# Optimization experiments

Measured on AMD Instinct MI355X. Metric: run time of the kernel, lower is better.

## Reference

```python
import jax, jax.numpy as jnp
import numpy as np

V, E, H, L = 32000, 512, 1024, 2
B, S, T = 32, 64, 64


def setup_inputs() -> dict:
    key = jax.random.key(0)
    ks = jax.random.split(key, 16)
    sd = 0.05
    p = lambda k, shape: (jax.random.normal(k, shape, jnp.float32) * sd)
    z = lambda shape: jnp.zeros(shape, jnp.float32)
    return {
        "tgt_batch": jax.random.randint(ks[0], (B, S), 0, V),
        "enc_h": p(ks[1], (L, B, H)),
        "enc_c": p(ks[2], (L, B, H)),
        "enc_outputs": p(ks[3], (T, B, H)),
        "emb": p(ks[4], (V, E)),
        "W_ih0": p(ks[5], (4 * H, E + H)),
        "W_hh0": p(ks[6], (4 * H, H)),
        "b_ih0": z((4 * H,)),
        "b_hh0": z((4 * H,)),
        "W_ih1": p(ks[7], (4 * H, H)),
        "W_hh1": p(ks[8], (4 * H, H)),
        "b_ih1": z((4 * H,)),
        "b_hh1": z((4 * H,)),
        "Wa": p(ks[9], (H, 2 * H)),
        "ba": z((H,)),
        "va": p(ks[10], (H,)),
        "Wc": p(ks[11], (H, 2 * H)),
        "bc": z((H,)),
        "Wo": p(ks[12], (V, H)),
        "bo": z((V,)),
        "teacher_forcing": 1,
    }


def _lstm_cell(x, h, c, Wih, Whh, bih, bhh):
    # PyTorch gate order: i, f, g, o
    g = x @ Wih.T + bih + h @ Whh.T + bhh
    i, f, gg, o = jnp.split(g, 4, axis=1)
    c2 = jax.nn.sigmoid(f) * c + jax.nn.sigmoid(i) * jnp.tanh(gg)
    return jax.nn.sigmoid(o) * jnp.tanh(c2), c2


def reference(tgt_batch, enc_h, enc_c, enc_outputs, emb,
              W_ih0, W_hh0, b_ih0, b_hh0, W_ih1, W_hh1, b_ih1, b_hh1,
              Wa, ba, va, Wc, bc, Wo, bo, teacher_forcing):
    # teacher_forcing == 1 -> always feed the gold previous word (matches
    # the torch loop, whose sampling branch is never taken at tf=1.0).
    tgt = tgt_batch.T  # [S, B], seq-first

    def step(carry, x_t):
        h, c, attn_h = carry  # h,c: [L,B,H]; attn_h: [B,H]
        x = jnp.concatenate([emb[x_t], attn_h], axis=1)  # [B, E+H]
        h0, c0 = _lstm_cell(x, h[0], c[0], W_ih0, W_hh0, b_ih0, b_hh0)
        h1, c1 = _lstm_cell(h0, h[1], c[1], W_ih1, W_hh1, b_ih1, b_hh1)
        # additive ('concat') attention over encoder states, query = top h
        hid = jnp.broadcast_to(h1[None], enc_outputs.shape)  # [T,B,H]
        energy = jnp.tanh(jnp.concatenate([hid, enc_outputs], axis=-1) @ Wa.T + ba)
        scores = jnp.einsum('tbh,h->bt', energy, va)  # [B,T]
        weights = jax.nn.softmax(scores, axis=1)
        context = jnp.einsum('bt,tbh->bh', weights, enc_outputs)  # [B,H]
        attn_h2 = jnp.tanh(jnp.concatenate([h1, context], axis=1) @ Wc.T + bc)
        logp = jax.nn.log_softmax(attn_h2 @ Wo.T + bo, axis=1)  # [B,V]
        return (jnp.stack([h0, h1]), jnp.stack([c0, c1]), attn_h2), logp

    init = (enc_h, enc_c, jnp.zeros((tgt.shape[1], H), enc_h.dtype))
    _, dec_outputs = jax.lax.scan(step, init, tgt[:-1])  # [S-1, B, V]
    dec_output_words = jnp.argmax(dec_outputs, axis=-1).astype(jnp.int32)
    return dec_outputs, dec_output_words
```

## Files before the change

kernel.cpp:

```cpp
#include <hip/hip_runtime.h>
#include <math.h>

#define VOCAB 32000
#define EMBD  512
#define HID   1024
#define BATCH 32
#define SEQ   64
#define TENC  64
#define NSTEP 63
#define G4    4096

typedef __attribute__((ext_vector_type(8))) short short8;
typedef __attribute__((ext_vector_type(4))) float f32x4;
typedef __attribute__((ext_vector_type(4))) unsigned short us4;
typedef unsigned short u16;

__device__ __forceinline__ float4 ld4(const float* p) {
  return *reinterpret_cast<const float4*>(p);
}
__device__ __forceinline__ u16 f2bf(float x) {
  unsigned u = __float_as_uint(x);
  return (u16)((u + 0x7fffu + ((u >> 16) & 1u)) >> 16);
}
__device__ __forceinline__ float bf2f(u16 h) {
  return __uint_as_float(((unsigned)h) << 16);
}

template<int MODE>
__device__ __forceinline__ void mfma32(
    const u16* __restrict__ Xahi, const u16* __restrict__ Xalo,
    const u16* __restrict__ Xbhi, const u16* __restrict__ Xblo,
    const u16* __restrict__ Whi,  const u16* __restrict__ Wlo,
    int nt, float* res)
{
  const int tid = threadIdx.x;
  const int w = tid >> 6, l = tid & 63;
  const int c = l & 15, koct = l >> 4;
  constexpr int K   = (MODE == 0) ? 2048 : 1024;
  constexpr int WS  = (MODE == 0) ? 2048 : 1024;
  constexpr int SPW = K / 32 / 4;
  const int r0 = c, r1 = 16 + c;
  const int wr0 = (MODE == 0) ? ((r0 >> 3)*1024 + nt*8 + (r0 & 7)) : (nt*32 + r0);
  const int wr1 = (MODE == 0) ? ((r1 >> 3)*1024 + nt*8 + (r1 & 7)) : (nt*32 + r1);
  const u16* bh0 = Whi + (size_t)wr0 * WS;
  const u16* bh1 = Whi + (size_t)wr1 * WS;
  const u16* bl0 = Wlo + (size_t)wr0 * WS;
  const u16* bl1 = Wlo + (size_t)wr1 * WS;

  auto ldA = [&](int m, int kg, int lo) -> short8 {
    const u16* base;
    if (MODE == 0 && kg >= 1024) base = lo ? Xblo : Xbhi;
    else                         base = lo ? Xalo : Xahi;
    const int b = m*16 + c;
    return *reinterpret_cast<const short8*>(base + b*1024 + (kg & 1023));
  };

  f32x4 acc[2][2];
  #pragma unroll
  for (int m = 0; m < 2; ++m)
    #pragma unroll
    for (int n = 0; n < 2; ++n) acc[m][n] = (f32x4){0.f,0.f,0.f,0.f};

  const int s0 = w * SPW;
  short8 Ah[2], Al[2], Bh[2], Bl[2];
  {
    const int kg = s0*32 + koct*8;
    Ah[0]=ldA(0,kg,0); Ah[1]=ldA(1,kg,0); Al[0]=ldA(0,kg,1); Al[1]=ldA(1,kg,1);
    Bh[0]=*reinterpret_cast<const short8*>(bh0+kg);
    Bh[1]=*reinterpret_cast<const short8*>(bh1+kg);
    Bl[0]=*reinterpret_cast<const short8*>(bl0+kg);
    Bl[1]=*reinterpret_cast<const short8*>(bl1+kg);
  }
  for (int s = s0; s < s0 + SPW; ++s) {
    short8 nAh[2], nAl[2], nBh[2], nBl[2];
    if (s + 1 < s0 + SPW) {
      const int kg = (s+1)*32 + koct*8;
      nAh[0]=ldA(0,kg,0); nAh[1]=ldA(1,kg,0); nAl[0]=ldA(0,kg,1); nAl[1]=ldA(1,kg,1);
      nBh[0]=*reinterpret_cast<const short8*>(bh0+kg);
      nBh[1]=*reinterpret_cast<const short8*>(bh1+kg);
      nBl[0]=*reinterpret_cast<const short8*>(bl0+kg);
      nBl[1]=*reinterpret_cast<const short8*>(bl1+kg);
    }
    #pragma unroll
    for (int n = 0; n < 2; ++n)
      #pragma unroll
      for (int m = 0; m < 2; ++m) {
        acc[m][n] = __builtin_amdgcn_mfma_f32_16x16x32_bf16(Ah[m], Bh[n], acc[m][n], 0, 0, 0);
        acc[m][n] = __builtin_amdgcn_mfma_f32_16x16x32_bf16(Ah[m], Bl[n], acc[m][n], 0, 0, 0);
        acc[m][n] = __builtin_amdgcn_mfma_f32_16x16x32_bf16(Al[m], Bh[n], acc[m][n], 0, 0, 0);
      }
    #pragma unroll
    for (int i = 0; i < 2; ++i) { Ah[i]=nAh[i]; Al[i]=nAl[i]; Bh[i]=nBh[i]; Bl[i]=nBl[i]; }
  }
  #pragma unroll
  for (int m = 0; m < 2; ++m)
    #pragma unroll
    for (int n = 0; n < 2; ++n)
      #pragma unroll
      for (int r = 0; r < 4; ++r) {
        const int b = m*16 + koct*4 + r;
        const int rr = n*16 + c;
        res[w*1056 + b*33 + rr] = acc[m][n][r];
      }
}

struct GKM {
  const u16 *Xahi, *Xalo, *Xbhi, *Xblo;
  const u16 *Whi, *Wlo;
  const float* bsum; const float* gembt;
  float* c; u16 *hhi; u16 *hlo;
};

template<int HASGEMB>
__global__ __launch_bounds__(256) void gates_mfma_k(GKM P) {
  __shared__ float res[4*1056];
  mfma32<0>(P.Xahi, P.Xalo, P.Xbhi, P.Xblo, P.Whi, P.Wlo, blockIdx.x, res);
  __syncthreads();
  const int tid = threadIdx.x;
  const int b = tid >> 3, j = tid & 7;
  const int n = blockIdx.x*8 + j;
  float g4[4];
  #pragma unroll
  for (int g = 0; g < 4; ++g) {
    const int r = g*8 + j;
    float s = P.bsum[g*1024 + n]
            + res[b*33+r] + res[1056 + b*33+r] + res[2112 + b*33+r] + res[3168 + b*33+r];
    if (HASGEMB) s += P.gembt[(size_t)b*G4 + g*1024 + n];
    g4[g] = s;
  }
  const float si = 1.f/(1.f+expf(-g4[0]));
  const float sf = 1.f/(1.f+expf(-g4[1]));
  const float so = 1.f/(1.f+expf(-g4[3]));
  const int i = b*HID + n;
  const float cn = sf*P.c[i] + si*tanhf(g4[2]);
  P.c[i] = cn;
  const float h = so*tanhf(cn);
  const u16 hh = f2bf(h);
  P.hhi[i] = hh;
  P.hlo[i] = f2bf(h - bf2f(hh));
}

struct PKM {
  const u16 *Xhi, *Xlo; const u16 *Whi, *Wlo; float* Pq;
};

__global__ __launch_bounds__(256) void proj_mfma_k(PKM P) {
  __shared__ float res[4*1056];
  mfma32<1>(P.Xhi, P.Xlo, nullptr, nullptr, P.Whi, P.Wlo, blockIdx.x, res);
  __syncthreads();
  const int tid = threadIdx.x;
  #pragma unroll
  for (int q = 0; q < 4; ++q) {
    const int o = q*256 + tid;
    const int b = o >> 5, r = o & 31;
    const float s = res[b*33+r] + res[1056 + b*33+r]
                  + res[2112 + b*33+r] + res[3168 + b*33+r];
    P.Pq[(size_t)b*2048 + blockIdx.x*32 + r] = s;
  }
}

struct AKM {
  const float* Pq; const float* PreAC; const float* va; const float* bc;
  u16* AHthi; u16* AHtlo;
};

__global__ __launch_bounds__(1024) void attn_k(AKM P) {
  __shared__ float QS[HID];
  __shared__ float sw[TENC];
  __shared__ float W64[TENC];
  const int b = blockIdx.x;
  const int tid = threadIdx.x;
  QS[tid] = P.Pq[(size_t)b*2048 + tid];
  __syncthreads();
  const int lane = tid & 63, wid = tid >> 6;
  float vreg[16];
  #pragma unroll
  for (int i2 = 0; i2 < 16; ++i2) vreg[i2] = P.va[lane + 64*i2];
  #pragma unroll
  for (int j = 0; j < 4; ++j) {
    const int te = wid*4 + j;
    const float* pr = P.PreAC + ((size_t)te*BATCH + b)*2048;
    float s = 0.f;
    #pragma unroll
    for (int i2 = 0; i2 < 16; ++i2) {
      const int idx = lane + 64*i2;
      s += vreg[i2] * tanhf(QS[idx] + pr[idx]);
    }
    #pragma unroll
    for (int off = 32; off; off >>= 1) s += __shfl_xor(s, off);
    if (lane == 0) sw[te] = s;
  }
  __syncthreads();
  if (tid < TENC) {
    const float v = sw[tid];
    float mx = v;
    #pragma unroll
    for (int off = 32; off; off >>= 1) mx = fmaxf(mx, __shfl_xor(mx, off));
    const float e = expf(v - mx);
    float sum = e;
    #pragma unroll
    for (int off = 32; off; off >>= 1) sum += __shfl_xor(sum, off);
    W64[tid] = e / sum;
  }
  __syncthreads();
  const int hh = tid;
  float acc = 0.f;
  #pragma unroll 8
  for (int te = 0; te < TENC; ++te)
    acc += W64[te] * P.PreAC[((size_t)te*BATCH + b)*2048 + HID + hh];
  const float hc = P.Pq[(size_t)b*2048 + HID + hh] + P.bc[hh];
  const float ah = tanhf(acc + hc);
  const u16 ahh = f2bf(ah);
  P.AHthi[(size_t)b*HID + hh] = ahh;
  P.AHtlo[(size_t)b*HID + hh] = f2bf(ah - bf2f(ahh));
}

struct TM {
  const u16 *Ahi, *Alo, *Bhi, *Blo;
  const int* tgt; const float* bias;
  float* out; int ldc, M, ntile_n;
};

template<int NC, int AMODE>
__global__ __launch_bounds__(256) void tile_k(TM P) {
  __shared__ float smemf[6144];
  u16* sA = (u16*)smemf;
  u16* sB = sA + 4096;
  constexpr int K = NC * 32;
  const int tile = blockIdx.x;
  const int mi = tile / P.ntile_n, ni = tile % P.ntile_n;
  const int m0 = mi * 64, n0 = ni * 128;
  const int tid = threadIdx.x;
  const int w = tid >> 6, l = tid & 63;
  const int mb = (w & 1) * 32, nb = (w >> 1) * 64;
  f32x4 acc[2][4];
  #pragma unroll
  for (int mt = 0; mt < 2; ++mt)
    #pragma unroll
    for (int nt = 0; nt < 4; ++nt) acc[mt][nt] = (f32x4){0.f,0.f,0.f,0.f};

  const int arow = tid >> 2, akg = tid & 3;
  const int brow = tid >> 1, bkg = (tid & 1) * 2;
  size_t arbase;
  if (AMODE == 1) {
    const int row = m0 + arow;
    const int tok = P.tgt[(row & 31)*SEQ + (row >> 5)];
    arbase = (size_t)tok * K;
  } else {
    arbase = (size_t)(m0 + arow) * K;
  }
  const size_t brbase = (size_t)(n0 + brow) * K;

  short8 pah, pal, pbh0, pbh1, pbl0, pbl1;
  {
    const size_t ao = arbase + akg*8;
    const size_t bo0 = brbase + bkg*8;
    pah  = *reinterpret_cast<const short8*>(P.Ahi + ao);
    pal  = *reinterpret_cast<const short8*>(P.Alo + ao);
    pbh0 = *reinterpret_cast<const short8*>(P.Bhi + bo0);
    pbh1 = *reinterpret_cast<const short8*>(P.Bhi + bo0 + 8);
    pbl0 = *reinterpret_cast<const short8*>(P.Blo + bo0);
    pbl1 = *reinterpret_cast<const short8*>(P.Blo + bo0 + 8);
  }
  for (int kc = 0; kc < NC; ++kc) {
    __syncthreads();
    *reinterpret_cast<short8*>(sA + ((0*4 + akg)*64 + arow)*8) = pah;
    *reinterpret_cast<short8*>(sA + ((1*4 + akg)*64 + arow)*8) = pal;
    *reinterpret_cast<short8*>(sB + ((0*4 + bkg  )*128 + brow)*8) = pbh0;
    *reinterpret_cast<short8*>(sB + ((0*4 + bkg+1)*128 + brow)*8) = pbh1;
    *reinterpret_cast<short8*>(sB + ((1*4 + bkg  )*128 + brow)*8) = pbl0;
    *reinterpret_cast<short8*>(sB + ((1*4 + bkg+1)*128 + brow)*8) = pbl1;
    __syncthreads();
    if (kc + 1 < NC) {
      const size_t ao = arbase + (kc+1)*32 + akg*8;
      const size_t bo0 = brbase + (kc+1)*32 + bkg*8;
      pah  = *reinterpret_cast<const short8*>(P.Ahi + ao);
      pal  = *reinterpret_cast<const short8*>(P.Alo + ao);
      pbh0 = *reinterpret_cast<const short8*>(P.Bhi + bo0);
      pbh1 = *reinterpret_cast<const short8*>(P.Bhi + bo0 + 8);
      pbl0 = *reinterpret_cast<const short8*>(P.Blo + bo0);
      pbl1 = *reinterpret_cast<const short8*>(P.Blo + bo0 + 8);
    }
    const int kg = l >> 4, rr = l & 15;
    short8 ah[2], al[2];
    #pragma unroll
    for (int mt = 0; mt < 2; ++mt) {
      ah[mt] = *reinterpret_cast<const short8*>(sA + ((0*4 + kg)*64 + mb + mt*16 + rr)*8);
      al[mt] = *reinterpret_cast<const short8*>(sA + ((1*4 + kg)*64 + mb + mt*16 + rr)*8);
    }
    #pragma unroll
    for (int nt = 0; nt < 4; ++nt) {
      const short8 bh = *reinterpret_cast<const short8*>(sB + ((0*4 + kg)*128 + nb + nt*16 + rr)*8);
      const short8 bl = *reinterpret_cast<const short8*>(sB + ((1*4 + kg)*128 + nb + nt*16 + rr)*8);
      #pragma unroll
      for (int mt = 0; mt < 2; ++mt) {
        acc[mt][nt] = __builtin_amdgcn_mfma_f32_16x16x32_bf16(ah[mt], bh, acc[mt][nt], 0, 0, 0);
        acc[mt][nt] = __builtin_amdgcn_mfma_f32_16x16x32_bf16(ah[mt], bl, acc[mt][nt], 0, 0, 0);
        acc[mt][nt] = __builtin_amdgcn_mfma_f32_16x16x32_bf16(al[mt], bh, acc[mt][nt], 0, 0, 0);
      }
    }
  }
  #pragma unroll
  for (int mt = 0; mt < 2; ++mt) {
    #pragma unroll
    for (int nt = 0; nt < 4; ++nt) {
      #pragma unroll
      for (int r = 0; r < 4; ++r) {
        const int row = m0 + mb + mt*16 + (l >> 4)*4 + r;
        const int col = n0 + nb + nt*16 + (l & 15);
        if (row < P.M) {
          const float bb = P.bias ? P.bias[col] : 0.f;
          P.out[(size_t)row*P.ldc + col] = acc[mt][nt][r] + bb;
        }
      }
    }
  }
}

template<int MODE>
__global__ __launch_bounds__(256) void pack_k(const float* __restrict__ A,
                                              const float* __restrict__ B,
                                              u16* __restrict__ hi, u16* __restrict__ lo) {
  constexpr int ROWS = (MODE == 2 || MODE == 3) ? 2048 : 4096;
  constexpr int K    = (MODE == 2 || MODE == 3) ? 1024 : (MODE == 4 ? 512 : 2048);
  const size_t total = (size_t)ROWS * (K/4);
  for (size_t i = (size_t)blockIdx.x*256 + threadIdx.x; i < total;
       i += (size_t)gridDim.x*256) {
    const int row = (int)(i / (K/4));
    const int k = (int)(i % (K/4)) * 4;
    float4 v;
    if (MODE == 0) v = (k < 1024) ? ld4(A + (size_t)row*1536 + 512 + k)
                                  : ld4(B + (size_t)row*1024 + (k - 1024));
    else if (MODE == 1) v = (k < 1024) ? ld4(A + (size_t)row*1024 + k)
                                       : ld4(B + (size_t)row*1024 + (k - 1024));
    else if (MODE == 2) v = (row < 1024) ? ld4(A + (size_t)row*2048 + k)
                                         : ld4(B + (size_t)(row - 1024)*2048 + k);
    else if (MODE == 3) v = (row < 1024) ? ld4(A + (size_t)row*2048 + 1024 + k)
                                         : ld4(B + (size_t)(row - 1024)*2048 + 1024 + k);
    else v = ld4(A + (size_t)row*1536 + k);
    us4 h, l;
    h.x = f2bf(v.x); l.x = f2bf(v.x - bf2f(h.x));
    h.y = f2bf(v.y); l.y = f2bf(v.y - bf2f(h.y));
    h.z = f2bf(v.z); l.z = f2bf(v.z - bf2f(h.z));
    h.w = f2bf(v.w); l.w = f2bf(v.w - bf2f(h.w));
    *reinterpret_cast<us4*>(hi + i*4) = h;
    *reinterpret_cast<us4*>(lo + i*4) = l;
  }
}

__global__ __launch_bounds__(256) void cvt_k(const float* __restrict__ src,
                                             u16* __restrict__ hi,
                                             u16* __restrict__ lo, int n) {
  int i = (blockIdx.x*256 + threadIdx.x) * 4;
  const int stride = gridDim.x * 256 * 4;
  for (; i < n; i += stride) {
    const float4 v = ld4(src + i);
    us4 h, l;
    h.x = f2bf(v.x); l.x = f2bf(v.x - bf2f(h.x));
    h.y = f2bf(v.y); l.y = f2bf(v.y - bf2f(h.y));
    h.z = f2bf(v.z); l.z = f2bf(v.z - bf2f(h.z));
    h.w = f2bf(v.w); l.w = f2bf(v.w - bf2f(h.w));
    *reinterpret_cast<us4*>(hi + i) = h;
    *reinterpret_cast<us4*>(lo + i) = l;
  }
}

struct WGP {
  const float* A; const float* W; const float* W2; const float* bias;
  const int* tgt; const float* emb;
  float* C; int ldc;
};

template<int WM>
__device__ __forceinline__ float4 ldWL(const WGP& P, int r, int k) {
  if (WM == 2) return ld4(P.W + (size_t)r * (EMBD + HID) + k);
  if (r < HID) return ld4(P.W  + (size_t)r * (2*HID) + HID + k);
  return ld4(P.W2 + (size_t)(r - HID) * (2*HID) + HID + k);
}

template<int WM>
__device__ __forceinline__ float4 ldAL(const WGP& P, int row, int k) {
  if (WM == 2) {
    const int tok = P.tgt[(row & 31) * SEQ + (row >> 5)];
    return ld4(P.emb + (size_t)tok * EMBD + k);
  }
  return ld4(P.A + (size_t)row * 1024 + k);
}

template<int WM>
__global__ __launch_bounds__(256, 2) void gemmL(WGP P) {
  constexpr int KK = (WM == 2) ? 512 : 1024;
  __shared__ float At[32*36];
  __shared__ float Wt[32*260];
  const int tid = threadIdx.x;
  const int m0 = blockIdx.x * 32;
  const int n0 = blockIdx.y * 256;
  const int lr = tid >> 3, lc = (tid & 7) << 2;
  const int tn = tid & 31, tm = tid >> 5;
  float acc[4][8];
  #pragma unroll
  for (int i = 0; i < 4; ++i)
    #pragma unroll
    for (int x = 0; x < 8; ++x) acc[i][x] = 0.f;

  float4 av = ldAL<WM>(P, m0 + lr, lc);
  float4 wv[8];
  #pragma unroll
  for (int it = 0; it < 8; ++it) wv[it] = ldWL<WM>(P, n0 + lr + it*32, lc);

  for (int k0 = 0; k0 < KK; k0 += 32) {
    float4 avn, wvn[8];
    if (k0 + 32 < KK) {
      avn = ldAL<WM>(P, m0 + lr, k0 + 32 + lc);
      #pragma unroll
      for (int it = 0; it < 8; ++it) wvn[it] = ldWL<WM>(P, n0 + lr + it*32, k0 + 32 + lc);
    }
    __syncthreads();
    At[(lc+0)*36+lr]=av.x; At[(lc+1)*36+lr]=av.y; At[(lc+2)*36+lr]=av.z; At[(lc+3)*36+lr]=av.w;
    #pragma unroll
    for (int it = 0; it < 8; ++it) {
      const int r = lr + it*32;
      Wt[(lc+0)*260+r]=wv[it].x; Wt[(lc+1)*260+r]=wv[it].y;
      Wt[(lc+2)*260+r]=wv[it].z; Wt[(lc+3)*260+r]=wv[it].w;
    }
    __syncthreads();
    #pragma unroll
    for (int kk = 0; kk < 32; ++kk) {
      const float4 a  = *reinterpret_cast<const float4*>(&At[kk*36 + tm*4]);
      const float4 w0 = *reinterpret_cast<const float4*>(&Wt[kk*260 + tn*8]);
      const float4 w1 = *reinterpret_cast<const float4*>(&Wt[kk*260 + tn*8 + 4]);
      #pragma unroll
      for (int i = 0; i < 4; ++i) {
        const float ai = (&a.x)[i];
        acc[i][0]+=ai*w0.x; acc[i][1]+=ai*w0.y; acc[i][2]+=ai*w0.z; acc[i][3]+=ai*w0.w;
        acc[i][4]+=ai*w1.x; acc[i][5]+=ai*w1.y; acc[i][6]+=ai*w1.z; acc[i][7]+=ai*w1.w;
      }
    }
    av = avn;
    #pragma unroll
    for (int it = 0; it < 8; ++it) wv[it] = wvn[it];
  }
  const int na = n0 + tn*8, ma = m0 + tm*4;
  float bb[8];
  #pragma unroll
  for (int x = 0; x < 8; ++x) {
    if (WM == 1) bb[x] = (na + x < HID) ? P.bias[na+x] : 0.f;
    else         bb[x] = 0.f;
  }
  #pragma unroll
  for (int i = 0; i < 4; ++i)
    #pragma unroll
    for (int x = 0; x < 8; ++x)
      P.C[(size_t)(ma+i)*P.ldc + na + x] = acc[i][x] + bb[x];
}

__global__ __launch_bounds__(512) void lsm_k(float* __restrict__ out,
                                             float* __restrict__ words) {
  const int b = blockIdx.x;
  const int t = blockIdx.y;
  float* row = out + ((size_t)t*BATCH + b)*VOCAB;
  const int tid = threadIdx.x;
  float m = -INFINITY, s = 0.f; int mi = 0;
  for (int v = tid; v < VOCAB; v += 512) {
    const float x = row[v];
    if (x > m) { s = s * expf(m - x) + 1.f; m = x; mi = v; }
    else s += expf(x - m);
  }
  __shared__ float sm[512]; __shared__ float sv[512]; __shared__ int si[512];
  sm[tid] = m; sv[tid] = s; si[tid] = mi;
  __syncthreads();
  for (int st = 256; st; st >>= 1) {
    if (tid < st) {
      const float om = sm[tid+st], os = sv[tid+st]; const int oi = si[tid+st];
      if (om > sm[tid]) {
        sv[tid] = os + sv[tid] * expf(sm[tid] - om);
        sm[tid] = om; si[tid] = oi;
      } else if (om == sm[tid]) {
        sv[tid] += os;
        if (oi < si[tid]) si[tid] = oi;
      } else {
        sv[tid] += os * expf(om - sm[tid]);
      }
    }
    __syncthreads();
  }
  const float lse = logf(sv[0]) + sm[0];
  const int amax = si[0];
  for (int v = tid; v < VOCAB; v += 512) row[v] = row[v] - lse;
  if (tid == 0) words[(size_t)t*BATCH + b] = (float)amax;
}

__global__ __launch_bounds__(256) void init_k(const float* __restrict__ enc_h,
                                              const float* __restrict__ enc_c,
                                              const float* __restrict__ bih0,
                                              const float* __restrict__ bhh0,
                                              const float* __restrict__ bih1,
                                              const float* __restrict__ bhh1,
                                              const float* __restrict__ ba,
                                              float* c0, float* c1,
                                              u16* h0hi, u16* h0lo, u16* h1hi, u16* h1lo,
                                              u16* zahhi, u16* zahlo,
                                              float* bsum0, float* bsum1,
                                              float* bias2048) {
  const int i = blockIdx.x*256 + threadIdx.x;
  if (i < BATCH*HID) {
    c0[i] = enc_c[i]; c1[i] = enc_c[BATCH*HID + i];
    const float v0 = enc_h[i];
    const u16 h0 = f2bf(v0);
    h0hi[i] = h0; h0lo[i] = f2bf(v0 - bf2f(h0));
    const float v1 = enc_h[BATCH*HID + i];
    const u16 h1 = f2bf(v1);
    h1hi[i] = h1; h1lo[i] = f2bf(v1 - bf2f(h1));
    zahhi[i] = 0; zahlo[i] = 0;
  }
  if (i < G4) {
    bsum0[i] = bih0[i] + bhh0[i];
    bsum1[i] = bih1[i] + bhh1[i];
  }
  if (i < 2048) bias2048[i] = (i < HID) ? ba[i] : 0.f;
}

extern "C" void kernel_launch(void* const* d_in, const int* in_sizes, int n_in,
                              void* d_out, int out_size, void* d_ws, size_t ws_size,
                              hipStream_t stream) {
  const int*   tgt   = (const int*)d_in[0];
  const float* enc_h = (const float*)d_in[1];
  const float* enc_c = (const float*)d_in[2];
  const float* enc   = (const float*)d_in[3];
  const float* emb   = (const float*)d_in[4];
  const float* Wih0  = (const float*)d_in[5];
  const float* Whh0  = (const float*)d_in[6];
  const float* bih0  = (const float*)d_in[7];
  const float* bhh0  = (const float*)d_in[8];
  const float* Wih1  = (const float*)d_in[9];
  const float* Whh1  = (const float*)d_in[10];
  const float* bih1  = (const float*)d_in[11];
  const float* bhh1  = (const float*)d_in[12];
  const float* Wa    = (const float*)d_in[13];
  const float* ba    = (const float*)d_in[14];
  const float* va    = (const float*)d_in[15];
  const float* Wc    = (const float*)d_in[16];
  const float* bc    = (const float*)d_in[17];
  const float* Wo    = (const float*)d_in[18];
  const float* bo    = (const float*)d_in[19];

  char* base = (char*)d_ws;
  size_t cur = 0;
  auto take = [&](size_t bytes) { char* p = base + cur; cur = (cur + bytes + 63) & ~(size_t)63; return p; };

  u16* AHhi = (u16*)take((size_t)2048*1024*2);
  u16* AHlo = (u16*)take((size_t)2048*1024*2);
  float* PreAC = (float*)take((size_t)2048*2048*4);
  float* Gemb  = (float*)take((size_t)NSTEP*BATCH*G4*4);
  float* Pq    = (float*)take((size_t)BATCH*2048*4);
  float* c0    = (float*)take(BATCH*HID*4);
  float* c1v   = (float*)take(BATCH*HID*4);
  float* bsum0 = (float*)take(G4*4);
  float* bsum1 = (float*)take(G4*4);
  float* bias2048 = (float*)take(2048*4);
  u16* W0hi = (u16*)take((size_t)4096*2048*2);
  u16* W0lo = (u16*)take((size_t)4096*2048*2);
  u16* W1hi = (u16*)take((size_t)4096*2048*2);
  u16* W1lo = (u16*)take((size_t)4096*2048*2);
  u16* WAhi = (u16*)take((size_t)2048*1024*2);
  u16* WAlo = (u16*)take((size_t)2048*1024*2);
  u16* h0Ahi = (u16*)take(BATCH*HID*2);
  u16* h0Alo = (u16*)take(BATCH*HID*2);
  u16* h0Bhi = (u16*)take(BATCH*HID*2);
  u16* h0Blo = (u16*)take(BATCH*HID*2);
  u16* h1Ahi = (u16*)take(BATCH*HID*2);
  u16* h1Alo = (u16*)take(BATCH*HID*2);
  u16* h1Bhi = (u16*)take(BATCH*HID*2);
  u16* h1Blo = (u16*)take(BATCH*HID*2);
  u16* zahhi = (u16*)take(BATCH*HID*2);
  u16* zahlo = (u16*)take(BATCH*HID*2);
  char* S = take((size_t)VOCAB*1024*2*2);
  const bool fast = ws_size >= cur;

  u16* enchi = (u16*)S;
  u16* enclo = enchi + (size_t)2048*1024;
  u16* embhi = enclo + (size_t)2048*1024;
  u16* emblo = embhi + (size_t)VOCAB*EMBD;
  u16* WAChi = emblo + (size_t)VOCAB*EMBD;
  u16* WAClo = WAChi + (size_t)2048*1024;
  u16* W0ehi = WAClo + (size_t)2048*1024;
  u16* W0elo = W0ehi + (size_t)4096*512;
  u16* Wohi = fast ? (u16*)S : (u16*)PreAC;
  u16* Wolo = Wohi + (size_t)VOCAB*1024;

  float* out   = (float*)d_out;
  float* words = out + (size_t)NSTEP*BATCH*VOCAB;

  init_k<<<dim3(128), 256, 0, stream>>>(enc_h, enc_c, bih0, bhh0, bih1, bhh1, ba,
                                        c0, c1v, h0Ahi, h0Alo, h1Ahi, h1Alo,
                                        zahhi, zahlo, bsum0, bsum1, bias2048);

  if (fast) {
    cvt_k<<<dim3(512), 256, 0, stream>>>(enc, enchi, enclo, 2048*1024);
    cvt_k<<<dim3(4096), 256, 0, stream>>>(emb, embhi, emblo, VOCAB*EMBD);
    pack_k<3><<<dim3(512), 256, 0, stream>>>(Wa, Wc, WAChi, WAClo);
    pack_k<4><<<dim3(512), 256, 0, stream>>>(Wih0, nullptr, W0ehi, W0elo);
    {
      TM p; p.Ahi = enchi; p.Alo = enclo; p.Bhi = WAChi; p.Blo = WAClo;
      p.tgt = nullptr; p.bias = bias2048; p.out = PreAC;
      p.ldc = 2048; p.M = 2048; p.ntile_n = 16;
      tile_k<32,0><<<dim3(512), 256, 0, stream>>>(p);
    }
    {
      TM p; p.Ahi = embhi; p.Alo = emblo; p.Bhi = W0ehi; p.Blo = W0elo;
      p.tgt = tgt; p.bias = nullptr; p.out = Gemb;
      p.ldc = G4; p.M = NSTEP*BATCH; p.ntile_n = 32;
      tile_k<16,1><<<dim3(1024), 256, 0, stream>>>(p);
    }
  } else {
    { WGP p = {}; p.A = enc; p.W = Wa; p.W2 = Wc; p.bias = ba; p.C = PreAC; p.ldc = 2048;
      gemmL<1><<<dim3(64, 8), 256, 0, stream>>>(p); }
    { WGP p = {}; p.W = Wih0; p.tgt = tgt; p.emb = emb; p.C = Gemb; p.ldc = G4;
      gemmL<2><<<dim3(NSTEP*BATCH/32, G4/256), 256, 0, stream>>>(p); }
  }
  pack_k<0><<<dim3(1024), 256, 0, stream>>>(Wih0, Whh0, W0hi, W0lo);
  pack_k<1><<<dim3(1024), 256, 0, stream>>>(Wih1, Whh1, W1hi, W1lo);
  pack_k<2><<<dim3(512), 256, 0, stream>>>(Wa, Wc, WAhi, WAlo);

  for (int t = 0; t < NSTEP; ++t) {
    const u16* ahphi = t ? (AHhi + (size_t)(t-1)*BATCH*HID) : zahhi;
    const u16* ahplo = t ? (AHlo + (size_t)(t-1)*BATCH*HID) : zahlo;
    const u16* h0phi = (t & 1) ? h0Bhi : h0Ahi;
    const u16* h0plo = (t & 1) ? h0Blo : h0Alo;
    u16* h0chi = (t & 1) ? h0Ahi : h0Bhi;
    u16* h0clo = (t & 1) ? h0Alo : h0Blo;
    const u16* h1phi = (t & 1) ? h1Bhi : h1Ahi;
    const u16* h1plo = (t & 1) ? h1Blo : h1Alo;
    u16* h1chi = (t & 1) ? h1Ahi : h1Bhi;
    u16* h1clo = (t & 1) ? h1Alo : h1Blo;

    {
      GKM p = {};
      p.Xahi = ahphi; p.Xalo = ahplo; p.Xbhi = h0phi; p.Xblo = h0plo;
      p.Whi = W0hi; p.Wlo = W0lo;
      p.bsum = bsum0; p.gembt = Gemb + (size_t)t*BATCH*G4;
      p.c = c0; p.hhi = h0chi; p.hlo = h0clo;
      gates_mfma_k<1><<<dim3(128), 256, 0, stream>>>(p);
    }
    {
      GKM p = {};
      p.Xahi = h0chi; p.Xalo = h0clo; p.Xbhi = h1phi; p.Xblo = h1plo;
      p.Whi = W1hi; p.Wlo = W1lo;
      p.bsum = bsum1; p.gembt = nullptr;
      p.c = c1v; p.hhi = h1chi; p.hlo = h1clo;
      gates_mfma_k<0><<<dim3(128), 256, 0, stream>>>(p);
    }
    {
      PKM p; p.Xhi = h1chi; p.Xlo = h1clo; p.Whi = WAhi; p.Wlo = WAlo; p.Pq = Pq;
      proj_mfma_k<<<dim3(64), 256, 0, stream>>>(p);
    }
    {
      AKM p; p.Pq = Pq; p.PreAC = PreAC; p.va = va; p.bc = bc;
      p.AHthi = AHhi + (size_t)t*BATCH*HID;
      p.AHtlo = AHlo + (size_t)t*BATCH*HID;
      attn_k<<<dim3(BATCH), 1024, 0, stream>>>(p);
    }
  }

  cvt_k<<<dim3(4096), 256, 0, stream>>>(Wo, Wohi, Wolo, VOCAB*1024);
  {
    TM p; p.Ahi = AHhi; p.Alo = AHlo; p.Bhi = Wohi; p.Blo = Wolo;
    p.tgt = nullptr; p.bias = bo; p.out = out;
    p.ldc = VOCAB; p.M = NSTEP*BATCH; p.ntile_n = 250;
    tile_k<32,0><<<dim3(8000), 256, 0, stream>>>(p);
  }
  lsm_k<<<dim3(BATCH, NSTEP), 512, 0, stream>>>(out, words);
}
```

Measured before the change: 6.062 ms.

## Split recurrent GEMM K-loop across 8 waves and merge prep kernels into one launch

The per-step gates and projection MFMA kernels now use 512 threads (8 waves) per block, splitting the K dimension across twice as many waves and reducing the partial sums from shared memory. This targets the latency-bound sequential recurrence, where only 128 or 64 blocks run per step, by raising per-block parallelism. Separately, the weight and activation conversion and packing kernels are merged into a single prep launch dispatched by block index, cutting launch count. The cost is more shared memory per block and a longer reduction step.

```diff
diff --git a/kernel.cpp b/kernel.cpp
--- a/kernel.cpp
+++ b/kernel.cpp
@@ -26,7 +26,7 @@
   return __uint_as_float(((unsigned)h) << 16);
 }
 
-template<int MODE>
+template<int MODE, int NW>
 __device__ __forceinline__ void mfma32(
     const u16* __restrict__ Xahi, const u16* __restrict__ Xalo,
     const u16* __restrict__ Xbhi, const u16* __restrict__ Xblo,
@@ -38,7 +38,7 @@
   const int c = l & 15, koct = l >> 4;
   constexpr int K   = (MODE == 0) ? 2048 : 1024;
   constexpr int WS  = (MODE == 0) ? 2048 : 1024;
-  constexpr int SPW = K / 32 / 4;
+  constexpr int SPW = K / 32 / NW;
   const int r0 = c, r1 = 16 + c;
   const int wr0 = (MODE == 0) ? ((r0 >> 3)*1024 + nt*8 + (r0 & 7)) : (nt*32 + r0);
   const int wr1 = (MODE == 0) ? ((r1 >> 3)*1024 + nt*8 + (r1 & 7)) : (nt*32 + r1);
@@ -112,49 +112,53 @@
 };
 
 template<int HASGEMB>
-__global__ __launch_bounds__(256) void gates_mfma_k(GKM P) {
-  __shared__ float res[4*1056];
-  mfma32<0>(P.Xahi, P.Xalo, P.Xbhi, P.Xblo, P.Whi, P.Wlo, blockIdx.x, res);
+__global__ __launch_bounds__(512) void gates_mfma_k(GKM P) {
+  __shared__ float res[8*1056];
+  mfma32<0,8>(P.Xahi, P.Xalo, P.Xbhi, P.Xblo, P.Whi, P.Wlo, blockIdx.x, res);
   __syncthreads();
   const int tid = threadIdx.x;
-  const int b = tid >> 3, j = tid & 7;
-  const int n = blockIdx.x*8 + j;
-  float g4[4];
-  #pragma unroll
-  for (int g = 0; g < 4; ++g) {
-    const int r = g*8 + j;
-    float s = P.bsum[g*1024 + n]
-            + res[b*33+r] + res[1056 + b*33+r] + res[2112 + b*33+r] + res[3168 + b*33+r];
-    if (HASGEMB) s += P.gembt[(size_t)b*G4 + g*1024 + n];
-    g4[g] = s;
-  }
-  const float si = 1.f/(1.f+expf(-g4[0]));
-  const float sf = 1.f/(1.f+expf(-g4[1]));
-  const float so = 1.f/(1.f+expf(-g4[3]));
-  const int i = b*HID + n;
-  const float cn = sf*P.c[i] + si*tanhf(g4[2]);
-  P.c[i] = cn;
-  const float h = so*tanhf(cn);
-  const u16 hh = f2bf(h);
-  P.hhi[i] = hh;
-  P.hlo[i] = f2bf(h - bf2f(hh));
+  if (tid < 256) {
+    const int b = tid >> 3, j = tid & 7;
+    const int n = blockIdx.x*8 + j;
+    float g4[4];
+    #pragma unroll
+    for (int g = 0; g < 4; ++g) {
+      const int r = g*8 + j;
+      float s = P.bsum[g*1024 + n];
+      #pragma unroll
+      for (int w = 0; w < 8; ++w) s += res[w*1056 + b*33 + r];
+      if (HASGEMB) s += P.gembt[(size_t)b*G4 + g*1024 + n];
+      g4[g] = s;
+    }
+    const float si = 1.f/(1.f+expf(-g4[0]));
+    const float sf = 1.f/(1.f+expf(-g4[1]));
+    const float so = 1.f/(1.f+expf(-g4[3]));
+    const int i = b*HID + n;
+    const float cn = sf*P.c[i] + si*tanhf(g4[2]);
+    P.c[i] = cn;
+    const float h = so*tanhf(cn);
+    const u16 hh = f2bf(h);
+    P.hhi[i] = hh;
+    P.hlo[i] = f2bf(h - bf2f(hh));
+  }
 }
 
 struct PKM {
   const u16 *Xhi, *Xlo; const u16 *Whi, *Wlo; float* Pq;
 };
 
-__global__ __launch_bounds__(256) void proj_mfma_k(PKM P) {
-  __shared__ float res[4*1056];
-  mfma32<1>(P.Xhi, P.Xlo, nullptr, nullptr, P.Whi, P.Wlo, blockIdx.x, res);
+__global__ __launch_bounds__(512) void proj_mfma_k(PKM P) {
+  __shared__ float res[8*1056];
+  mfma32<1,8>(P.Xhi, P.Xlo, nullptr, nullptr, P.Whi, P.Wlo, blockIdx.x, res);
   __syncthreads();
   const int tid = threadIdx.x;
   #pragma unroll
-  for (int q = 0; q < 4; ++q) {
-    const int o = q*256 + tid;
+  for (int q = 0; q < 2; ++q) {
+    const int o = q*512 + tid;
     const int b = o >> 5, r = o & 31;
-    const float s = res[b*33+r] + res[1056 + b*33+r]
-                  + res[2112 + b*33+r] + res[3168 + b*33+r];
+    float s = 0.f;
+    #pragma unroll
+    for (int w = 0; w < 8; ++w) s += res[w*1056 + b*33 + r];
     P.Pq[(size_t)b*2048 + blockIdx.x*32 + r] = s;
   }
 }
@@ -317,15 +321,32 @@
   }
 }
 
+__device__ __forceinline__ void cvt_body(const float* __restrict__ src,
+                                         u16* __restrict__ hi, u16* __restrict__ lo,
+                                         int n, int bid, int nblk) {
+  int i = (bid*256 + (int)threadIdx.x) * 4;
+  const int stride = nblk * 256 * 4;
+  for (; i < n; i += stride) {
+    const float4 v = ld4(src + i);
+    us4 h, l;
+    h.x = f2bf(v.x); l.x = f2bf(v.x - bf2f(h.x));
+    h.y = f2bf(v.y); l.y = f2bf(v.y - bf2f(h.y));
+    h.z = f2bf(v.z); l.z = f2bf(v.z - bf2f(h.z));
+    h.w = f2bf(v.w); l.w = f2bf(v.w - bf2f(h.w));
+    *reinterpret_cast<us4*>(hi + i) = h;
+    *reinterpret_cast<us4*>(lo + i) = l;
+  }
+}
+
 template<int MODE>
-__global__ __launch_bounds__(256) void pack_k(const float* __restrict__ A,
-                                              const float* __restrict__ B,
-                                              u16* __restrict__ hi, u16* __restrict__ lo) {
+__device__ __forceinline__ void pk_body(const float* __restrict__ A,
+                                        const float* __restrict__ B,
+                                        u16* __restrict__ hi, u16* __restrict__ lo,
+                                        int bid, int nblk) {
   constexpr int ROWS = (MODE == 2 || MODE == 3) ? 2048 : 4096;
   constexpr int K    = (MODE == 2 || MODE == 3) ? 1024 : (MODE == 4 ? 512 : 2048);
   const size_t total = (size_t)ROWS * (K/4);
-  for (size_t i = (size_t)blockIdx.x*256 + threadIdx.x; i < total;
-       i += (size_t)gridDim.x*256) {
+  for (size_t i = (size_t)bid*256 + threadIdx.x; i < total; i += (size_t)nblk*256) {
     const int row = (int)(i / (K/4));
     const int k = (int)(i % (K/4)) * 4;
     float4 v;
@@ -348,21 +369,34 @@
   }
 }
 
+struct PrepP {
+  const float *enc, *emb, *Wa, *Wc, *Wih0, *Whh0, *Wih1, *Whh1;
+  u16 *enchi,*enclo,*embhi,*emblo,*WAChi,*WAClo,*W0ehi,*W0elo;
+  u16 *W0hi,*W0lo,*W1hi,*W1lo,*WAhi,*WAlo;
+};
+
+template<int FAST>
+__global__ __launch_bounds__(256) void prep_k(PrepP P) {
+  const int bid = blockIdx.x;
+  if (FAST) {
+    if      (bid < 256)  cvt_body(P.enc, P.enchi, P.enclo, 2048*1024, bid, 256);
+    else if (bid < 2304) cvt_body(P.emb, P.embhi, P.emblo, VOCAB*EMBD, bid-256, 2048);
+    else if (bid < 2560) pk_body<3>(P.Wa, P.Wc, P.WAChi, P.WAClo, bid-2304, 256);
+    else if (bid < 2816) pk_body<4>(P.Wih0, nullptr, P.W0ehi, P.W0elo, bid-2560, 256);
+    else if (bid < 3840) pk_body<0>(P.Wih0, P.Whh0, P.W0hi, P.W0lo, bid-2816, 1024);
+    else if (bid < 4864) pk_body<1>(P.Wih1, P.Whh1, P.W1hi, P.W1lo, bid-3840, 1024);
+    else                 pk_body<2>(P.Wa, P.Wc, P.WAhi, P.WAlo, bid-4864, 256);
+  } else {
+    if      (bid < 1024) pk_body<0>(P.Wih0, P.Whh0, P.W0hi, P.W0lo, bid, 1024);
+    else if (bid < 2048) pk_body<1>(P.Wih1, P.Whh1, P.W1hi, P.W1lo, bid-1024, 1024);
+    else                 pk_body<2>(P.Wa, P.Wc, P.WAhi, P.WAlo, bid-2048, 256);
+  }
+}
+
 __global__ __launch_bounds__(256) void cvt_k(const float* __restrict__ src,
                                              u16* __restrict__ hi,
                                              u16* __restrict__ lo, int n) {
-  int i = (blockIdx.x*256 + threadIdx.x) * 4;
-  const int stride = gridDim.x * 256 * 4;
-  for (; i < n; i += stride) {
-    const float4 v = ld4(src + i);
-    us4 h, l;
-    h.x = f2bf(v.x); l.x = f2bf(v.x - bf2f(h.x));
-    h.y = f2bf(v.y); l.y = f2bf(v.y - bf2f(h.y));
-    h.z = f2bf(v.z); l.z = f2bf(v.z - bf2f(h.z));
-    h.w = f2bf(v.w); l.w = f2bf(v.w - bf2f(h.w));
-    *reinterpret_cast<us4*>(hi + i) = h;
-    *reinterpret_cast<us4*>(lo + i) = l;
-  }
+  cvt_body(src, hi, lo, n, blockIdx.x, gridDim.x);
 }
 
 struct WGP {
@@ -595,11 +629,19 @@
                                         c0, c1v, h0Ahi, h0Alo, h1Ahi, h1Alo,
                                         zahhi, zahlo, bsum0, bsum1, bias2048);
 
+  {
+    PrepP p;
+    p.enc = enc; p.emb = emb; p.Wa = Wa; p.Wc = Wc;
+    p.Wih0 = Wih0; p.Whh0 = Whh0; p.Wih1 = Wih1; p.Whh1 = Whh1;
+    p.enchi = enchi; p.enclo = enclo; p.embhi = embhi; p.emblo = emblo;
+    p.WAChi = WAChi; p.WAClo = WAClo; p.W0ehi = W0ehi; p.W0elo = W0elo;
+    p.W0hi = W0hi; p.W0lo = W0lo; p.W1hi = W1hi; p.W1lo = W1lo;
+    p.WAhi = WAhi; p.WAlo = WAlo;
+    if (fast) prep_k<1><<<dim3(5120), 256, 0, stream>>>(p);
+    else      prep_k<0><<<dim3(2304), 256, 0, stream>>>(p);
+  }
+
   if (fast) {
-    cvt_k<<<dim3(512), 256, 0, stream>>>(enc, enchi, enclo, 2048*1024);
-    cvt_k<<<dim3(4096), 256, 0, stream>>>(emb, embhi, emblo, VOCAB*EMBD);
-    pack_k<3><<<dim3(512), 256, 0, stream>>>(Wa, Wc, WAChi, WAClo);
-    pack_k<4><<<dim3(512), 256, 0, stream>>>(Wih0, nullptr, W0ehi, W0elo);
     {
       TM p; p.Ahi = enchi; p.Alo = enclo; p.Bhi = WAChi; p.Blo = WAClo;
       p.tgt = nullptr; p.bias = bias2048; p.out = PreAC;
@@ -618,9 +660,6 @@
     { WGP p = {}; p.W = Wih0; p.tgt = tgt; p.emb = emb; p.C = Gemb; p.ldc = G4;
       gemmL<2><<<dim3(NSTEP*BATCH/32, G4/256), 256, 0, stream>>>(p); }
   }
-  pack_k<0><<<dim3(1024), 256, 0, stream>>>(Wih0, Whh0, W0hi, W0lo);
-  pack_k<1><<<dim3(1024), 256, 0, stream>>>(Wih1, Whh1, W1hi, W1lo);
-  pack_k<2><<<dim3(512), 256, 0, stream>>>(Wa, Wc, WAhi, WAlo);
 
   for (int t = 0; t < NSTEP; ++t) {
     const u16* ahphi = t ? (AHhi + (size_t)(t-1)*BATCH*HID) : zahhi;
@@ -640,7 +679,7 @@
       p.Whi = W0hi; p.Wlo = W0lo;
       p.bsum = bsum0; p.gembt = Gemb + (size_t)t*BATCH*G4;
       p.c = c0; p.hhi = h0chi; p.hlo = h0clo;
-      gates_mfma_k<1><<<dim3(128), 256, 0, stream>>>(p);
+      gates_mfma_k<1><<<dim3(128), 512, 0, stream>>>(p);
     }
     {
       GKM p = {};
@@ -648,11 +687,11 @@
       p.Whi = W1hi; p.Wlo = W1lo;
       p.bsum = bsum1; p.gembt = nullptr;
       p.c = c1v; p.hhi = h1chi; p.hlo = h1clo;
-      gates_mfma_k<0><<<dim3(128), 256, 0, stream>>>(p);
+      gates_mfma_k<0><<<dim3(128), 512, 0, stream>>>(p);
     }
     {
       PKM p; p.Xhi = h1chi; p.Xlo = h1clo; p.Whi = WAhi; p.Wlo = WAlo; p.Pq = Pq;
-      proj_mfma_k<<<dim3(64), 256, 0, stream>>>(p);
+      proj_mfma_k<<<dim3(64), 512, 0, stream>>>(p);
     }
     {
       AKM p; p.Pq = Pq; p.PreAC = PreAC; p.va = va; p.bc = bc;
```

Measured after the change: 6.000 ms. No clear change (-1.0%).
